# Optimization experiments

Measured on AMD Instinct MI355X. Metric: run time of the kernel, lower is better.

The kernel has to match this reference:

```python
import jax, jax.numpy as jnp
import numpy as np

ALPHA = 0.1
EPS = 1e-7

def proj(x):
    # Re-project onto hyperboloid: time coord t = sqrt(1 + |s|^2)
    s = x[:, 1:]
    t = jnp.sqrt(1.0 + jnp.sum(s * s, axis=-1, keepdims=True))
    return jnp.concatenate([t, s], axis=-1)

def linner(x, y):
    # Lorentzian inner product <x,y>_L = -x0*y0 + <xs, ys>
    return -x[..., 0] * y[..., 0] + jnp.sum(x[..., 1:] * y[..., 1:], axis=-1)

def safe_acosh(z):
    return jnp.arccosh(jnp.maximum(z, 1.0 + EPS))

def setup_inputs() -> dict:
    key = jax.random.key(0)
    k1, k2 = jax.random.split(key)
    B, n, A = 1_000_000, 64, 16
    s = jax.random.normal(k1, (B, n), dtype=jnp.float32) * 0.5
    t = jnp.sqrt(1.0 + jnp.sum(s * s, axis=-1, keepdims=True))
    hyp_emb = jnp.concatenate([t, s], axis=-1)  # [B, n+1] on hyperboloid
    a_s = jax.random.normal(k2, (A, n), dtype=jnp.float32) * 0.01
    a_t = jnp.sqrt(1.0 + jnp.sum(a_s * a_s, axis=-1, keepdims=True))
    anchors = jnp.concatenate([a_t, a_s], axis=-1)  # [A, n+1]
    return {"hyp_emb": hyp_emb, "anchors": anchors}

def reference(hyp_emb, anchors):
    anchors_p = proj(anchors)  # [A, d]
    # Lorentzian pairwise inner products [B, A]
    inner = (-hyp_emb[:, :1] * anchors_p[None, :, 0]
             + jnp.einsum('bd,ad->ba', hyp_emb[:, 1:], anchors_p[:, 1:]))
    dists = safe_acosh(-inner)
    nearest_idx = jnp.argmin(dists, axis=1)        # [B]
    na = anchors_p[nearest_idx]                    # [B, d] gather
    # log_map_x(y): d(x,y) * (y + <x,y> x) / ||y + <x,y> x||_L
    xy = linner(hyp_emb, na)                       # [B]
    d = safe_acosh(-xy)
    u = na + xy[:, None] * hyp_emb
    unorm = jnp.sqrt(jnp.maximum(linner(u, u), EPS))
    v = (ALPHA * d / unorm)[:, None] * u           # alpha * direction
    # exp_map_x(v): cosh(|v|) x + sinh(|v|) v / |v|
    vn = jnp.sqrt(jnp.maximum(linner(v, v), EPS * EPS))
    sinhc = jnp.where(vn > EPS, jnp.sinh(vn) / vn, 1.0)
    out = jnp.cosh(vn)[:, None] * hyp_emb + sinhc[:, None] * v
    return out
```

## Files before the change

kernel.cpp:

```cpp
#include <hip/hip_runtime.h>
#include <math.h>
#include <stdint.h>

#define ALPHA 0.1f
#define EPS 1e-7f

constexpr int D = 65;
constexpr int A = 16;
constexpr int WPB = 4;
constexpr int TPB = WPB * 64;
constexpr int RPW = 64;
constexpr int WAVE_FLOATS = RPW * D;

__device__ __forceinline__ void async_cp16(const float* g, float* l) {
    __builtin_amdgcn_global_load_lds(
        (const __attribute__((address_space(1))) uint32_t*)(uintptr_t)g,
        (__attribute__((address_space(3))) uint32_t*)(uint32_t)(uintptr_t)l,
        16, 0, 0);
}
__device__ __forceinline__ void async_cp4(const float* g, float* l) {
    __builtin_amdgcn_global_load_lds(
        (const __attribute__((address_space(1))) uint32_t*)(uintptr_t)g,
        (__attribute__((address_space(3))) uint32_t*)(uint32_t)(uintptr_t)l,
        4, 0, 0);
}

__global__ void prep_anchors(const float* __restrict__ anchors,
                             float* __restrict__ ws) {
    __shared__ float s_a[A * D];
    int tid = threadIdx.x;
    for (int i = tid; i < A * D; i += blockDim.x) s_a[i] = anchors[i];
    __syncthreads();
    if (tid < A) {
        float s = 0.f;
        for (int j = 1; j < D; ++j) {
            float v = s_a[tid * D + j];
            s = fmaf(v, v, s);
        }
        s_a[tid * D] = sqrtf(1.f + s);
    }
    __syncthreads();
    for (int i = tid; i < A * D; i += blockDim.x) {
        int a = i / D, j = i % D;
        ws[j * A + a] = s_a[i];
        ws[A * D + i] = s_a[i];
    }
}

__global__ __launch_bounds__(TPB, 2) void
homeo_kernel(const float* __restrict__ x,
             const float* __restrict__ aT,
             const float* __restrict__ aRM,
             float* __restrict__ out, int B, int nWG) {
    __shared__ float xs[WPB * WAVE_FLOATS];
    __shared__ float anch[A * D];

    const int tid = threadIdx.x;
    const int wave = tid >> 6;
    const int lane = tid & 63;
    const int wg = blockIdx.x * WPB + wave;
    const bool active = wg < nWG;

    float* lbase = xs + wave * WAVE_FLOATS;
    const long rowStart = (long)wg * RPW;
    const int nRows = active ? (int)min((long)RPW, (long)B - rowStart) : 0;

    if (active && nRows == RPW) {
        const float* gbase = x + rowStart * D;
#pragma unroll
        for (int c = 0; c < 16; ++c)
            async_cp16(gbase + c * 256 + lane * 4, lbase + c * 256);
        async_cp4(gbase + 16 * 256 + lane, lbase + 16 * 256);
    } else if (active && lane < nRows) {
        for (int j = 0; j < D; ++j)
            lbase[lane * D + j] = x[(rowStart + lane) * D + j];
    }

    for (int i = tid; i < A * D; i += TPB) anch[i] = aRM[i];
    __syncthreads();

    if (active && lane < nRows) {
        float xr[D];
#pragma unroll
        for (int j = 0; j < D; ++j) xr[j] = lbase[lane * D + j];

        float acc[A];
#pragma unroll
        for (int a = 0; a < A; ++a) acc[a] = -xr[0] * aT[a];
#pragma unroll
        for (int j = 1; j < D; ++j) {
            const float xj = xr[j];
#pragma unroll
            for (int a = 0; a < A; ++a)
                acc[a] = fmaf(xj, aT[j * A + a], acc[a]);
        }

        const float onePlusEps = 1.0f + EPS;
        float bestZ = fmaxf(-acc[0], onePlusEps);
        float xy = acc[0];
        int bidx = 0;
#pragma unroll
        for (int a = 1; a < A; ++a) {
            float z = fmaxf(-acc[a], onePlusEps);
            if (z < bestZ) { bestZ = z; bidx = a; xy = acc[a]; }
        }
        const float d = acoshf(bestZ);

        float nar[D];
#pragma unroll
        for (int j = 0; j < D; ++j) nar[j] = anch[bidx * D + j];

        float uu;
        {
            float u0 = fmaf(xy, xr[0], nar[0]);
            uu = -u0 * u0;
        }
#pragma unroll
        for (int j = 1; j < D; ++j) {
            float uj = fmaf(xy, xr[j], nar[j]);
            uu = fmaf(uj, uj, uu);
        }
        const float unorm = sqrtf(fmaxf(uu, EPS));
        const float c = ALPHA * d / unorm;
        const float vv = c * c * uu;
        const float vn = sqrtf(fmaxf(vv, EPS * EPS));
        const float sinhc = (vn > EPS) ? (sinhf(vn) / vn) : 1.0f;
        const float ch = coshf(vn);
        const float sc = sinhc * c;

#pragma unroll
        for (int j = 0; j < D; ++j) {
            float uj = fmaf(xy, xr[j], nar[j]);
            lbase[lane * D + j] = fmaf(ch, xr[j], sc * uj);
        }
    }

    asm volatile("s_waitcnt lgkmcnt(0)" ::: "memory");

    if (active && nRows == RPW) {
        float4* o4 = (float4*)(out + rowStart * D);
        const float4* l4 = (const float4*)lbase;
#pragma unroll
        for (int c = 0; c < 16; ++c) o4[c * 64 + lane] = l4[c * 64 + lane];
        out[rowStart * D + 16 * 256 + lane] = lbase[16 * 256 + lane];
    } else if (active && lane < nRows) {
        for (int j = 0; j < D; ++j)
            out[(rowStart + lane) * D + j] = lbase[lane * D + j];
    }
}

extern "C" void kernel_launch(void* const* d_in, const int* in_sizes, int n_in,
                              void* d_out, int out_size, void* d_ws, size_t ws_size,
                              hipStream_t stream) {
    const float* hyp = (const float*)d_in[0];
    const float* anchors = (const float*)d_in[1];
    float* out = (float*)d_out;
    float* ws = (float*)d_ws;

    const int B = in_sizes[0] / D;
    const int nWG = (B + RPW - 1) / RPW;
    const int grid = (nWG + WPB - 1) / WPB;

    prep_anchors<<<1, 256, 0, stream>>>(anchors, ws);
    homeo_kernel<<<grid, TPB, 0, stream>>>(hyp, ws, ws + A * D, out, B, nWG);
}
```

Measured before the change: 441.6 us.

## Use persistent single-wave blocks with double-buffered async LDS tile prefetch

Replaces the one-tile-per-wave launch with a fixed grid of single-wave persistent blocks that loop over tiles. The next tile is prefetched into a second LDS buffer via global_load_lds while the current one is computed, and the anchor table is loaded once per block. The output expression is also folded algebraically into k1*x + sc*na, which saves a per-element multiply. In exchange, occupancy is capped at a few waves per CU, and correctness depends on the hand-tuned vmcnt wait count.

```diff
diff --git a/kernel.cpp b/kernel.cpp
--- a/kernel.cpp
+++ b/kernel.cpp
@@ -7,10 +7,9 @@
 
 constexpr int D = 65;
 constexpr int A = 16;
-constexpr int WPB = 4;
-constexpr int TPB = WPB * 64;
 constexpr int RPW = 64;
-constexpr int WAVE_FLOATS = RPW * D;
+constexpr int TILE_FLOATS = RPW * D;
+constexpr int NBLOCKS = 1024;
 
 __device__ __forceinline__ void async_cp16(const float* g, float* l) {
     __builtin_amdgcn_global_load_lds(
@@ -47,105 +46,122 @@
     }
 }
 
-__global__ __launch_bounds__(TPB, 2) void
+__device__ __forceinline__ void row_math(const float xr[D],
+                                         const float* __restrict__ aT,
+                                         const float* __restrict__ anch,
+                                         float* __restrict__ orow) {
+    float acc[A];
+#pragma unroll
+    for (int a = 0; a < A; ++a) acc[a] = -xr[0] * aT[a];
+#pragma unroll
+    for (int j = 1; j < D; ++j) {
+        const float xj = xr[j];
+#pragma unroll
+        for (int a = 0; a < A; ++a)
+            acc[a] = fmaf(xj, aT[j * A + a], acc[a]);
+    }
+
+    const float onePlusEps = 1.0f + EPS;
+    float bestZ = fmaxf(-acc[0], onePlusEps);
+    float xy = acc[0];
+    int bidx = 0;
+#pragma unroll
+    for (int a = 1; a < A; ++a) {
+        float z = fmaxf(-acc[a], onePlusEps);
+        if (z < bestZ) { bestZ = z; bidx = a; xy = acc[a]; }
+    }
+    const float d = acoshf(bestZ);
+
+    const float* na = anch + bidx * D;
+    float uu;
+    {
+        float u0 = fmaf(xy, xr[0], na[0]);
+        uu = -u0 * u0;
+    }
+#pragma unroll
+    for (int j = 1; j < D; ++j) {
+        float uj = fmaf(xy, xr[j], na[j]);
+        uu = fmaf(uj, uj, uu);
+    }
+    const float unorm = sqrtf(fmaxf(uu, EPS));
+    const float c = ALPHA * d / unorm;
+    const float vv = c * c * uu;
+    const float vn = sqrtf(fmaxf(vv, EPS * EPS));
+    const float sinhc = (vn > EPS) ? (sinhf(vn) / vn) : 1.0f;
+    const float ch = coshf(vn);
+    const float sc = sinhc * c;
+    const float k1 = fmaf(sc, xy, ch);
+#pragma unroll
+    for (int j = 0; j < D; ++j)
+        orow[j] = fmaf(k1, xr[j], sc * na[j]);
+}
+
+__global__ __launch_bounds__(64, 1) void
 homeo_kernel(const float* __restrict__ x,
              const float* __restrict__ aT,
              const float* __restrict__ aRM,
-             float* __restrict__ out, int B, int nWG) {
-    __shared__ float xs[WPB * WAVE_FLOATS];
+             float* __restrict__ out, int B) {
+    __shared__ float buf[2][TILE_FLOATS];
     __shared__ float anch[A * D];
 
-    const int tid = threadIdx.x;
-    const int wave = tid >> 6;
-    const int lane = tid & 63;
-    const int wg = blockIdx.x * WPB + wave;
-    const bool active = wg < nWG;
+    const int lane = threadIdx.x;
+    const long stride = gridDim.x;
+    const int nTiles = (B + RPW - 1) / RPW;
 
-    float* lbase = xs + wave * WAVE_FLOATS;
-    const long rowStart = (long)wg * RPW;
-    const int nRows = active ? (int)min((long)RPW, (long)B - rowStart) : 0;
+    for (int i = lane; i < A * D; i += 64) anch[i] = aRM[i];
 
-    if (active && nRows == RPW) {
-        const float* gbase = x + rowStart * D;
+    {
+        const long t0 = blockIdx.x;
+        if (t0 < nTiles && (t0 + 1) * (long)RPW <= (long)B) {
+            const float* g = x + t0 * (long)TILE_FLOATS;
 #pragma unroll
-        for (int c = 0; c < 16; ++c)
-            async_cp16(gbase + c * 256 + lane * 4, lbase + c * 256);
-        async_cp4(gbase + 16 * 256 + lane, lbase + 16 * 256);
-    } else if (active && lane < nRows) {
-        for (int j = 0; j < D; ++j)
-            lbase[lane * D + j] = x[(rowStart + lane) * D + j];
+            for (int c = 0; c < 16; ++c)
+                async_cp16(g + c * 256 + lane * 4, buf[0] + c * 256);
+            async_cp4(g + 16 * 256 + lane, buf[0] + 16 * 256);
+        }
     }
-
-    for (int i = tid; i < A * D; i += TPB) anch[i] = aRM[i];
     __syncthreads();
 
-    if (active && lane < nRows) {
-        float xr[D];
+    int p = 0;
+    for (long t = blockIdx.x; t < nTiles; t += stride, p ^= 1) {
+        const long rowStart = t * RPW;
+        const int nRows = (int)min((long)RPW, (long)B - rowStart);
+
+        {
+            const long tn = t + stride;
+            if (tn < nTiles && (tn + 1) * (long)RPW <= (long)B) {
+                const float* g = x + tn * (long)TILE_FLOATS;
+                float* l = buf[p ^ 1];
 #pragma unroll
-        for (int j = 0; j < D; ++j) xr[j] = lbase[lane * D + j];
+                for (int c = 0; c < 16; ++c)
+                    async_cp16(g + c * 256 + lane * 4, l + c * 256);
+                async_cp4(g + 16 * 256 + lane, l + 16 * 256);
+            }
+        }
+        asm volatile("s_waitcnt vmcnt(17)" ::: "memory");
 
-        float acc[A];
+        float* lbase = buf[p];
+        if (nRows == RPW) {
+            float xr[D];
 #pragma unroll
-        for (int a = 0; a < A; ++a) acc[a] = -xr[0] * aT[a];
+            for (int j = 0; j < D; ++j) xr[j] = lbase[lane * D + j];
+
+            row_math(xr, aT, anch, lbase + lane * D);
+
+            asm volatile("s_waitcnt lgkmcnt(0)" ::: "memory");
+
+            float4* o4 = (float4*)(out + rowStart * (long)D);
+            const float4* l4 = (const float4*)lbase;
 #pragma unroll
-        for (int j = 1; j < D; ++j) {
-            const float xj = xr[j];
-#pragma unroll
-            for (int a = 0; a < A; ++a)
-                acc[a] = fmaf(xj, aT[j * A + a], acc[a]);
+            for (int c2 = 0; c2 < 16; ++c2)
+                o4[c2 * 64 + lane] = l4[c2 * 64 + lane];
+            out[rowStart * (long)D + 16 * 256 + lane] = lbase[16 * 256 + lane];
+        } else if (lane < nRows) {
+            const float* xg = x + (rowStart + lane) * (long)D;
+            float xr[D];
+            for (int j = 0; j < D; ++j) xr[j] = xg[j];
+            row_math(xr, aT, anch, out + (rowStart + lane) * (long)D);
         }
-
-        const float onePlusEps = 1.0f + EPS;
-        float bestZ = fmaxf(-acc[0], onePlusEps);
-        float xy = acc[0];
-        int bidx = 0;
-#pragma unroll
-        for (int a = 1; a < A; ++a) {
-            float z = fmaxf(-acc[a], onePlusEps);
-            if (z < bestZ) { bestZ = z; bidx = a; xy = acc[a]; }
-        }
-        const float d = acoshf(bestZ);
-
-        float nar[D];
-#pragma unroll
-        for (int j = 0; j < D; ++j) nar[j] = anch[bidx * D + j];
-
-        float uu;
-        {
-            float u0 = fmaf(xy, xr[0], nar[0]);
-            uu = -u0 * u0;
-        }
-#pragma unroll
-        for (int j = 1; j < D; ++j) {
-            float uj = fmaf(xy, xr[j], nar[j]);
-            uu = fmaf(uj, uj, uu);
-        }
-        const float unorm = sqrtf(fmaxf(uu, EPS));
-        const float c = ALPHA * d / unorm;
-        const float vv = c * c * uu;
-        const float vn = sqrtf(fmaxf(vv, EPS * EPS));
-        const float sinhc = (vn > EPS) ? (sinhf(vn) / vn) : 1.0f;
-        const float ch = coshf(vn);
-        const float sc = sinhc * c;
-
-#pragma unroll
-        for (int j = 0; j < D; ++j) {
-            float uj = fmaf(xy, xr[j], nar[j]);
-            lbase[lane * D + j] = fmaf(ch, xr[j], sc * uj);
-        }
-    }
-
-    asm volatile("s_waitcnt lgkmcnt(0)" ::: "memory");
-
-    if (active && nRows == RPW) {
-        float4* o4 = (float4*)(out + rowStart * D);
-        const float4* l4 = (const float4*)lbase;
-#pragma unroll
-        for (int c = 0; c < 16; ++c) o4[c * 64 + lane] = l4[c * 64 + lane];
-        out[rowStart * D + 16 * 256 + lane] = lbase[16 * 256 + lane];
-    } else if (active && lane < nRows) {
-        for (int j = 0; j < D; ++j)
-            out[(rowStart + lane) * D + j] = lbase[lane * D + j];
     }
 }
 
@@ -158,9 +174,9 @@
     float* ws = (float*)d_ws;
 
     const int B = in_sizes[0] / D;
-    const int nWG = (B + RPW - 1) / RPW;
-    const int grid = (nWG + WPB - 1) / WPB;
+    const int nTiles = (B + RPW - 1) / RPW;
+    const int grid = nTiles < NBLOCKS ? nTiles : NBLOCKS;
 
     prep_anchors<<<1, 256, 0, stream>>>(anchors, ws);
-    homeo_kernel<<<grid, TPB, 0, stream>>>(hyp, ws, ws + A * D, out, B, nWG);
+    homeo_kernel<<<grid, 64, 0, stream>>>(hyp, ws, ws + A * D, out, B);
 }
```

After: 445.6 us. Within noise of the previous version (+0.9%).
